# Kernel tuning notes

Measured on AMD Instinct MI355X. Metric: run time of the kernel, lower is better.

## Reference

```python
import jax, jax.numpy as jnp
import numpy as np

EPS = 1e-8  # torch CosineSimilarity eps


def setup_inputs() -> dict:
    key = jax.random.key(0)
    ks = jax.random.split(key, 7)
    B, N, T, C, M, MEM, IN, E = 8, 512, 64, 128, 32, 20, 2, 4
    s = 0.05  # keep softmax logits in a sane range (xavier-like scale)
    return {
        "input": jax.random.normal(ks[0], (B, N, T, IN), jnp.float32),
        "hidden": jax.random.normal(ks[1], (E, B, N, T, C), jnp.float32),
        "memory": jax.random.normal(ks[2], (MEM, M), jnp.float32) * s,
        "input_query": jax.random.normal(ks[3], (IN, M), jnp.float32) * s,
        "Wq": jax.random.normal(ks[4], (E, C, M), jnp.float32) * s,
        "Wk": jax.random.normal(ks[5], (E, C, M), jnp.float32) * s,
        "Wv": jax.random.normal(ks[6], (E, C, M), jnp.float32) * s,
    }


def _cosine_sim(a, b):
    # torch.nn.CosineSimilarity(dim=-1): dot / (max(||a||,eps)*max(||b||,eps))
    num = jnp.sum(a * b, axis=-1)
    na = jnp.maximum(jnp.linalg.norm(a, axis=-1), EPS)
    nb = jnp.maximum(jnp.linalg.norm(b, axis=-1), EPS)
    return num / (na * nb)


def reference(input, hidden, memory, input_query, Wq, Wk, Wv):
    B, N, T, _ = input.shape
    out_dim = 1
    # query_mem: soft read from memory bank -> [B,N,T,mem_hid]
    q_in = jnp.einsum("bnti,im->bntm", input, input_query)
    mem_score = jax.nn.softmax(jnp.einsum("bntm,km->bntk", q_in, memory), axis=-1)
    memories = jnp.einsum("bntk,km->bntm", mem_score, memory)
    # per-expert self-attention over T (vectorized over the 4 experts)
    q = jnp.einsum("ebntc,ecm->ebntm", hidden, Wq)
    k = jnp.einsum("ebntc,ecm->ebntm", hidden, Wk)
    v = jnp.einsum("ebntc,ecm->ebntm", hidden, Wv)
    energy = jnp.einsum("ebntm,ebnsm->ebnts", q, k)  # [E,B,N,T,T]
    att = jnp.einsum("ebnts,ebnsm->ebntm", jax.nn.softmax(energy, axis=-1), v)
    # cosine similarity of memory read vs each expert's attended hidden
    scores = _cosine_sim(memories[None], att)  # [E,B,N,T]
    scores = jnp.moveaxis(scores, 0, -1)  # [B,N,T,E]
    out = jnp.broadcast_to(scores[..., None, :], (B, N, T, out_dim, scores.shape[-1]))
    return out
```

## Files before the change

kernel.cpp:

```cpp
#include <hip/hip_runtime.h>
#include <hip/hip_bf16.h>
#include <math.h>

#define Bc 8
#define Nc 512
#define Tc 64
#define Cc 128
#define Mc 32
#define MEMc 20
#define Ec 4

#define LDK  40
#define LDVT 72

typedef short bf16x8 __attribute__((ext_vector_type(8)));
typedef float f32x4  __attribute__((ext_vector_type(4)));

__device__ __forceinline__ unsigned short f2bfu(float f) {
    return __builtin_bit_cast(unsigned short, __float2bfloat16(f));
}
__device__ __forceinline__ unsigned pk2bf(float x, float y) {
    return ((unsigned)f2bfu(y) << 16) | (unsigned)f2bfu(x);
}

__device__ __forceinline__ void gload_lds16(const void* g, void* l) {
    __builtin_amdgcn_global_load_lds(
        (const __attribute__((address_space(1))) unsigned int*)g,
        (__attribute__((address_space(3))) unsigned int*)l, 16, 0, 0);
}

__global__ void prep(const float* __restrict__ Wq, const float* __restrict__ Wk,
                     const float* __restrict__ Wv, const float* __restrict__ membank,
                     const float* __restrict__ iq,
                     short* __restrict__ wt_img, short* __restrict__ bankM,
                     float* __restrict__ G2) {
    const int t = threadIdx.x;
    if (blockIdx.x < 192) {
        int idx = blockIdx.x * 256 + t;
        int e   = idx / 12288;
        int r   = idx - e * 12288;
        int mat = r >> 12;
        int m   = (r >> 7) & 31;
        int c   = r & 127;
        const float* W = (mat == 0) ? Wq : (mat == 1) ? Wk : Wv;
        const int dst = e * 12288 + mat * 4096 + m * 128 + (c ^ ((m & 7) << 3));
        wt_img[dst] = (short)f2bfu(W[((size_t)e * Cc + c) * Mc + m]);
    } else {
        for (int idx = t; idx < Mc * 32; idx += 256) {
            int m = idx >> 5, k = idx & 31;
            bankM[idx] = (short)f2bfu((k < MEMc) ? membank[k * Mc + m] : 0.f);
        }
        if (t < MEMc) {
            float g0 = 0.f, g1 = 0.f;
            for (int m = 0; m < Mc; ++m) {
                float b = membank[t * Mc + m];
                g0 = fmaf(iq[m], b, g0);
                g1 = fmaf(iq[Mc + m], b, g1);
            }
            G2[2 * t]     = g0;
            G2[2 * t + 1] = g1;
        }
    }
}

__global__ __launch_bounds__(256, 4) void mg_mfma(
    const float* __restrict__ input,
    const float* __restrict__ hidden,
    const short* __restrict__ wt_img,
    const short* __restrict__ bankM,
    const float* __restrict__ G2,
    float* __restrict__ out)
{
    __shared__ __align__(16) short sh_wt[12288];
    __shared__ __align__(16) short sh_k [Tc * LDK];
    __shared__ __align__(16) short sh_vt[Mc * LDVT];

    const int t    = threadIdx.x;
    const int w    = t >> 6;
    const int lane = t & 63;
    const int lo   = lane & 15;
    const int hi   = lane >> 4;
    const int bn   = blockIdx.x & 4095;
    const int e    = blockIdx.x >> 12;

    {
        const short* gsrc = wt_img + (size_t)e * 12288 + w * 512 + lane * 8;
        short* ldst = sh_wt + w * 512;
        #pragma unroll
        for (int c = 0; c < 6; ++c)
            gload_lds16(gsrc + c * 2048, ldst + c * 2048);
    }

    float4 h4[8];
    {
        const float* hrow = hidden + (((size_t)(e * 4096 + bn)) * Tc + w * 16 + lo) * Cc + hi * 8;
        #pragma unroll
        for (int kt = 0; kt < 4; ++kt) {
            h4[2 * kt]     = *(const float4*)(hrow + kt * 32);
            h4[2 * kt + 1] = *(const float4*)(hrow + kt * 32 + 4);
        }
    }
    const float2 in2 = *(const float2*)(input + ((size_t)bn * Tc + lane) * 2);

    unsigned pd[10];
    #pragma unroll
    for (int kp = 0; kp < 10; ++kp) {
        const float4 g = *(const float4*)(G2 + 4 * kp);
        pd[kp] = pk2bf(__expf(in2.x * g.x + in2.y * g.y),
                       __expf(in2.x * g.z + in2.y * g.w));
    }

    bf16x8 a[4];
    #pragma unroll
    for (int kt = 0; kt < 4; ++kt) {
        const float4 x = h4[2 * kt], y = h4[2 * kt + 1];
        uint4 u = (uint4){pk2bf(x.x, x.y), pk2bf(x.z, x.w), pk2bf(y.x, y.y), pk2bf(y.z, y.w)};
        a[kt] = __builtin_bit_cast(bf16x8, u);
    }

    __syncthreads();

    f32x4 q_[2], k_[2], v_[2];
    #pragma unroll
    for (int nt = 0; nt < 2; ++nt) {
        q_[nt] = (f32x4){0.f, 0.f, 0.f, 0.f};
        k_[nt] = (f32x4){0.f, 0.f, 0.f, 0.f};
        v_[nt] = (f32x4){0.f, 0.f, 0.f, 0.f};
    }
    {
        const int swz = (lo & 7) << 3;
        int col[4];
        #pragma unroll
        for (int kt = 0; kt < 4; ++kt) col[kt] = (kt * 32 + hi * 8) ^ swz;
        const short* wrow = sh_wt + lo * 128;
        #pragma unroll
        for (int nt = 0; nt < 2; ++nt) {
            const short* p0 = wrow + nt * 2048;
            #pragma unroll
            for (int kt = 0; kt < 4; ++kt) {
                const bf16x8 aq = *(const bf16x8*)(p0 + col[kt]);
                const bf16x8 ak = *(const bf16x8*)(p0 + 4096 + col[kt]);
                const bf16x8 av = *(const bf16x8*)(p0 + 8192 + col[kt]);
                q_[nt] = __builtin_amdgcn_mfma_f32_16x16x32_bf16(aq, a[kt], q_[nt], 0, 0, 0);
                k_[nt] = __builtin_amdgcn_mfma_f32_16x16x32_bf16(ak, a[kt], k_[nt], 0, 0, 0);
                v_[nt] = __builtin_amdgcn_mfma_f32_16x16x32_bf16(av, a[kt], v_[nt], 0, 0, 0);
            }
        }
    }
    unsigned q_pk[4];
    #pragma unroll
    for (int nt = 0; nt < 2; ++nt) {
        uint2 kw = (uint2){pk2bf(k_[nt][0], k_[nt][1]), pk2bf(k_[nt][2], k_[nt][3])};
        *(uint2*)&sh_k[(w * 16 + lo) * LDK + nt * 16 + hi * 4] = kw;
        #pragma unroll
        for (int j = 0; j < 4; ++j)
            sh_vt[(nt * 16 + hi * 4 + j) * LDVT + w * 16 + lo] = (short)f2bfu(v_[nt][j]);
        q_pk[nt * 2]     = pk2bf(q_[nt][0], q_[nt][1]);
        q_pk[nt * 2 + 1] = pk2bf(q_[nt][2], q_[nt][3]);
    }

    f32x4 am[2];
    am[0] = (f32x4){0.f, 0.f, 0.f, 0.f};
    am[1] = (f32x4){0.f, 0.f, 0.f, 0.f};
    {
        const int addrD = (w * 16 + lo) * 4;
        unsigned Wd[10];
        #pragma unroll
        for (int u = 0; u < 10; ++u)
            Wd[u] = __builtin_amdgcn_ds_bpermute(addrD, (int)pd[u]);
        unsigned b2w[4];
        #pragma unroll
        for (int u = 0; u < 4; ++u) {
            const unsigned lo01 = (hi == 0) ? Wd[u] : Wd[4 + u];
            const unsigned hi23 = (u < 2) ? ((hi == 2) ? Wd[8 + u] : 0u) : 0u;
            b2w[u] = (hi < 2) ? lo01 : hi23;
        }
        const bf16x8 bp2 = __builtin_bit_cast(bf16x8, (uint4){b2w[0], b2w[1], b2w[2], b2w[3]});
        #pragma unroll
        for (int nt = 0; nt < 2; ++nt) {
            const bf16x8 ab = *(const bf16x8*)(bankM + (nt * 16 + lo) * 32 + hi * 8);
            am[nt] = __builtin_amdgcn_mfma_f32_16x16x32_bf16(ab, bp2, am[nt], 0, 0, 0);
        }
    }

    __syncthreads();

    unsigned pw[4][2];
    {
        const int A01 = (((hi & 1) * 32) + lo) << 2;
        const int A23 = A01 + 64;
        unsigned qb0, qb1, qb2, qb3;
        {
            unsigned l0 = __builtin_amdgcn_ds_bpermute(A01, (int)q_pk[0]);
            unsigned h0 = __builtin_amdgcn_ds_bpermute(A01, (int)q_pk[2]);
            unsigned l1 = __builtin_amdgcn_ds_bpermute(A01, (int)q_pk[1]);
            unsigned h1 = __builtin_amdgcn_ds_bpermute(A01, (int)q_pk[3]);
            unsigned l2 = __builtin_amdgcn_ds_bpermute(A23, (int)q_pk[0]);
            unsigned h2 = __builtin_amdgcn_ds_bpermute(A23, (int)q_pk[2]);
            unsigned l3 = __builtin_amdgcn_ds_bpermute(A23, (int)q_pk[1]);
            unsigned h3 = __builtin_amdgcn_ds_bpermute(A23, (int)q_pk[3]);
            qb0 = (hi < 2) ? l0 : h0;
            qb1 = (hi < 2) ? l1 : h1;
            qb2 = (hi < 2) ? l2 : h2;
            qb3 = (hi < 2) ? l3 : h3;
        }
        const bf16x8 bq = __builtin_bit_cast(bf16x8, (uint4){qb0, qb1, qb2, qb3});

        #pragma unroll
        for (int st = 0; st < 4; ++st) {
            const bf16x8 akf = *(const bf16x8*)&sh_k[(st * 16 + lo) * LDK + hi * 8];
            const f32x4 en = __builtin_amdgcn_mfma_f32_16x16x32_bf16(
                akf, bq, (f32x4){0.f, 0.f, 0.f, 0.f}, 0, 0, 0);
            pw[st][0] = pk2bf(__expf(en[0]), __expf(en[1]));
            pw[st][1] = pk2bf(__expf(en[2]), __expf(en[3]));
        }
    }

    f32x4 av[2];
    av[0] = (f32x4){0.f, 0.f, 0.f, 0.f};
    av[1] = (f32x4){0.f, 0.f, 0.f, 0.f};
    {
        const int addrA = (((hi & 1) * 2 + 0) * 16 + lo) * 4;
        const int addrB = (((hi & 1) * 2 + 1) * 16 + lo) * 4;
        bf16x8 bp[2];
        #pragma unroll
        for (int kt = 0; kt < 2; ++kt) {
            unsigned wrd[4];
            #pragma unroll
            for (int u = 0; u < 4; ++u) {
                const int adr = (u < 2) ? addrA : addrB;
                const unsigned ev = __builtin_amdgcn_ds_bpermute(adr, (int)pw[2 * kt][u & 1]);
                const unsigned od = __builtin_amdgcn_ds_bpermute(adr, (int)pw[2 * kt + 1][u & 1]);
                wrd[u] = (hi < 2) ? ev : od;
            }
            bp[kt] = __builtin_bit_cast(bf16x8, (uint4){wrd[0], wrd[1], wrd[2], wrd[3]});
        }
        #pragma unroll
        for (int nt = 0; nt < 2; ++nt)
            #pragma unroll
            for (int kt = 0; kt < 2; ++kt) {
                const bf16x8 avt = *(const bf16x8*)&sh_vt[(nt * 16 + lo) * LDVT + kt * 32 + hi * 8];
                av[nt] = __builtin_amdgcn_mfma_f32_16x16x32_bf16(avt, bp[kt], av[nt], 0, 0, 0);
            }
    }

    {
        float d = 0.f, na = 0.f, nb = 0.f;
        #pragma unroll
        for (int nt = 0; nt < 2; ++nt)
            #pragma unroll
            for (int j = 0; j < 4; ++j) {
                const float av_ = av[nt][j], am_ = am[nt][j];
                d  = fmaf(av_, am_, d);
                na = fmaf(av_, av_, na);
                nb = fmaf(am_, am_, nb);
            }
        d  += __shfl_xor(d, 16);  d  += __shfl_xor(d, 32);
        na += __shfl_xor(na, 16); na += __shfl_xor(na, 32);
        nb += __shfl_xor(nb, 16); nb += __shfl_xor(nb, 32);
        if (hi == 0) {
            const float denom = fmaxf(sqrtf(na), 1e-8f) * fmaxf(sqrtf(nb), 1e-8f);
            out[((size_t)bn * Tc + w * 16 + lo) * Ec + e] = d / denom;
        }
    }
}

extern "C" void kernel_launch(void* const* d_in, const int* in_sizes, int n_in,
                              void* d_out, int out_size, void* d_ws, size_t ws_size,
                              hipStream_t stream) {
    const float* input   = (const float*)d_in[0];
    const float* hidden  = (const float*)d_in[1];
    const float* membank = (const float*)d_in[2];
    const float* iq      = (const float*)d_in[3];
    const float* Wq      = (const float*)d_in[4];
    const float* Wk      = (const float*)d_in[5];
    const float* Wv      = (const float*)d_in[6];
    float* out = (float*)d_out;

    short* wt_img = (short*)d_ws;
    short* bankM  = (short*)((char*)d_ws + 98304);
    float* G2     = (float*)((char*)d_ws + 100352);

    prep<<<193, 256, 0, stream>>>(Wq, Wk, Wv, membank, iq, wt_img, bankM, G2);
    mg_mfma<<<Ec * Bc * Nc, 256, 0, stream>>>(input, hidden, wt_img, bankM, G2, out);
}
```

Measured before the change: 129.8 us.

## Process two (b,n) rows per block to amortize weight staging

Each block now handles two consecutive (b,n) positions for one expert, so the 24KB per-expert weight image loaded into LDS and the bankM fragments are reused across both. The grid is halved, shared K/V buffers are doubled, and launch bounds drop from 4 to 3 blocks per CU to make room for the larger register footprint. The aim is to cut the per-block weight load and launch overhead relative to the streamed hidden data. The cost is higher register pressure and lower occupancy.

```diff
diff --git a/kernel.cpp b/kernel.cpp
--- a/kernel.cpp
+++ b/kernel.cpp
@@ -63,7 +63,7 @@
     }
 }
 
-__global__ __launch_bounds__(256, 4) void mg_mfma(
+__global__ __launch_bounds__(256, 3) void mg_mfma(
     const float* __restrict__ input,
     const float* __restrict__ hidden,
     const short* __restrict__ wt_img,
@@ -72,16 +72,17 @@
     float* __restrict__ out)
 {
     __shared__ __align__(16) short sh_wt[12288];
-    __shared__ __align__(16) short sh_k [Tc * LDK];
-    __shared__ __align__(16) short sh_vt[Mc * LDVT];
+    __shared__ __align__(16) short sh_k [2][Tc * LDK];
+    __shared__ __align__(16) short sh_vt[2][Mc * LDVT];
 
     const int t    = threadIdx.x;
     const int w    = t >> 6;
     const int lane = t & 63;
     const int lo   = lane & 15;
     const int hi   = lane >> 4;
-    const int bn   = blockIdx.x & 4095;
-    const int e    = blockIdx.x >> 12;
+    const int e    = blockIdx.x >> 11;
+    const int bn0  = (blockIdx.x & 2047) * 2;
+    const int bn1  = bn0 + 1;
 
     {
         const short* gsrc = wt_img + (size_t)e * 12288 + w * 512 + lane * 8;
@@ -91,41 +92,80 @@
             gload_lds16(gsrc + c * 2048, ldst + c * 2048);
     }
 
-    float4 h4[8];
+    const float2 in2_0 = *(const float2*)(input + ((size_t)bn0 * Tc + lane) * 2);
+    const float2 in2_1 = *(const float2*)(input + ((size_t)bn1 * Tc + lane) * 2);
+    float4 h0[8], h1[8];
     {
-        const float* hrow = hidden + (((size_t)(e * 4096 + bn)) * Tc + w * 16 + lo) * Cc + hi * 8;
+        const float* hr0 = hidden + (((size_t)(e * 4096 + bn0)) * Tc + w * 16 + lo) * Cc + hi * 8;
+        const float* hr1 = hidden + (((size_t)(e * 4096 + bn1)) * Tc + w * 16 + lo) * Cc + hi * 8;
         #pragma unroll
         for (int kt = 0; kt < 4; ++kt) {
-            h4[2 * kt]     = *(const float4*)(hrow + kt * 32);
-            h4[2 * kt + 1] = *(const float4*)(hrow + kt * 32 + 4);
-        }
-    }
-    const float2 in2 = *(const float2*)(input + ((size_t)bn * Tc + lane) * 2);
-
-    unsigned pd[10];
+            h0[2 * kt]     = *(const float4*)(hr0 + kt * 32);
+            h0[2 * kt + 1] = *(const float4*)(hr0 + kt * 32 + 4);
+            h1[2 * kt]     = *(const float4*)(hr1 + kt * 32);
+            h1[2 * kt + 1] = *(const float4*)(hr1 + kt * 32 + 4);
+        }
+    }
+
+    unsigned pd0[10], pd1[10];
     #pragma unroll
     for (int kp = 0; kp < 10; ++kp) {
         const float4 g = *(const float4*)(G2 + 4 * kp);
-        pd[kp] = pk2bf(__expf(in2.x * g.x + in2.y * g.y),
-                       __expf(in2.x * g.z + in2.y * g.w));
-    }
-
-    bf16x8 a[4];
+        pd0[kp] = pk2bf(__expf(in2_0.x * g.x + in2_0.y * g.y),
+                        __expf(in2_0.x * g.z + in2_0.y * g.w));
+        pd1[kp] = pk2bf(__expf(in2_1.x * g.x + in2_1.y * g.y),
+                        __expf(in2_1.x * g.z + in2_1.y * g.w));
+    }
+
+    f32x4 am0[2], am1[2];
+    am0[0] = am0[1] = (f32x4){0.f, 0.f, 0.f, 0.f};
+    am1[0] = am1[1] = (f32x4){0.f, 0.f, 0.f, 0.f};
+    {
+        const int addrD = (w * 16 + lo) * 4;
+        unsigned W0[10], W1[10];
+        #pragma unroll
+        for (int u = 0; u < 10; ++u) {
+            W0[u] = __builtin_amdgcn_ds_bpermute(addrD, (int)pd0[u]);
+            W1[u] = __builtin_amdgcn_ds_bpermute(addrD, (int)pd1[u]);
+        }
+        unsigned b0[4], b1[4];
+        #pragma unroll
+        for (int u = 0; u < 4; ++u) {
+            const unsigned l0 = (hi == 0) ? W0[u] : W0[4 + u];
+            const unsigned h0_ = (u < 2) ? ((hi == 2) ? W0[8 + u] : 0u) : 0u;
+            b0[u] = (hi < 2) ? l0 : h0_;
+            const unsigned l1 = (hi == 0) ? W1[u] : W1[4 + u];
+            const unsigned h1_ = (u < 2) ? ((hi == 2) ? W1[8 + u] : 0u) : 0u;
+            b1[u] = (hi < 2) ? l1 : h1_;
+        }
+        const bf16x8 bp20 = __builtin_bit_cast(bf16x8, (uint4){b0[0], b0[1], b0[2], b0[3]});
+        const bf16x8 bp21 = __builtin_bit_cast(bf16x8, (uint4){b1[0], b1[1], b1[2], b1[3]});
+        #pragma unroll
+        for (int nt = 0; nt < 2; ++nt) {
+            const bf16x8 ab = *(const bf16x8*)(bankM + (nt * 16 + lo) * 32 + hi * 8);
+            am0[nt] = __builtin_amdgcn_mfma_f32_16x16x32_bf16(ab, bp20, am0[nt], 0, 0, 0);
+            am1[nt] = __builtin_amdgcn_mfma_f32_16x16x32_bf16(ab, bp21, am1[nt], 0, 0, 0);
+        }
+    }
+
+    bf16x8 a0[4], a1[4];
     #pragma unroll
     for (int kt = 0; kt < 4; ++kt) {
-        const float4 x = h4[2 * kt], y = h4[2 * kt + 1];
-        uint4 u = (uint4){pk2bf(x.x, x.y), pk2bf(x.z, x.w), pk2bf(y.x, y.y), pk2bf(y.z, y.w)};
-        a[kt] = __builtin_bit_cast(bf16x8, u);
+        const float4 x0 = h0[2 * kt], y0 = h0[2 * kt + 1];
+        a0[kt] = __builtin_bit_cast(bf16x8, (uint4){pk2bf(x0.x, x0.y), pk2bf(x0.z, x0.w),
+                                                    pk2bf(y0.x, y0.y), pk2bf(y0.z, y0.w)});
+        const float4 x1 = h1[2 * kt], y1 = h1[2 * kt + 1];
+        a1[kt] = __builtin_bit_cast(bf16x8, (uint4){pk2bf(x1.x, x1.y), pk2bf(x1.z, x1.w),
+                                                    pk2bf(y1.x, y1.y), pk2bf(y1.z, y1.w)});
     }
 
     __syncthreads();
 
-    f32x4 q_[2], k_[2], v_[2];
+    f32x4 q0_[2], k0_[2], v0_[2], q1_[2], k1_[2], v1_[2];
     #pragma unroll
     for (int nt = 0; nt < 2; ++nt) {
-        q_[nt] = (f32x4){0.f, 0.f, 0.f, 0.f};
-        k_[nt] = (f32x4){0.f, 0.f, 0.f, 0.f};
-        v_[nt] = (f32x4){0.f, 0.f, 0.f, 0.f};
+        q0_[nt] = k0_[nt] = v0_[nt] = (f32x4){0.f, 0.f, 0.f, 0.f};
+        q1_[nt] = k1_[nt] = v1_[nt] = (f32x4){0.f, 0.f, 0.f, 0.f};
     }
     {
         const int swz = (lo & 7) << 3;
@@ -138,113 +178,97 @@
             const short* p0 = wrow + nt * 2048;
             #pragma unroll
             for (int kt = 0; kt < 4; ++kt) {
-                const bf16x8 aq = *(const bf16x8*)(p0 + col[kt]);
-                const bf16x8 ak = *(const bf16x8*)(p0 + 4096 + col[kt]);
-                const bf16x8 av = *(const bf16x8*)(p0 + 8192 + col[kt]);
-                q_[nt] = __builtin_amdgcn_mfma_f32_16x16x32_bf16(aq, a[kt], q_[nt], 0, 0, 0);
-                k_[nt] = __builtin_amdgcn_mfma_f32_16x16x32_bf16(ak, a[kt], k_[nt], 0, 0, 0);
-                v_[nt] = __builtin_amdgcn_mfma_f32_16x16x32_bf16(av, a[kt], v_[nt], 0, 0, 0);
-            }
-        }
-    }
-    unsigned q_pk[4];
+                const bf16x8 wq = *(const bf16x8*)(p0 + col[kt]);
+                const bf16x8 wk = *(const bf16x8*)(p0 + 4096 + col[kt]);
+                const bf16x8 wv = *(const bf16x8*)(p0 + 8192 + col[kt]);
+                q0_[nt] = __builtin_amdgcn_mfma_f32_16x16x32_bf16(wq, a0[kt], q0_[nt], 0, 0, 0);
+                k0_[nt] = __builtin_amdgcn_mfma_f32_16x16x32_bf16(wk, a0[kt], k0_[nt], 0, 0, 0);
+                v0_[nt] = __builtin_amdgcn_mfma_f32_16x16x32_bf16(wv, a0[kt], v0_[nt], 0, 0, 0);
+                q1_[nt] = __builtin_amdgcn_mfma_f32_16x16x32_bf16(wq, a1[kt], q1_[nt], 0, 0, 0);
+                k1_[nt] = __builtin_amdgcn_mfma_f32_16x16x32_bf16(wk, a1[kt], k1_[nt], 0, 0, 0);
+                v1_[nt] = __builtin_amdgcn_mfma_f32_16x16x32_bf16(wv, a1[kt], v1_[nt], 0, 0, 0);
+            }
+        }
+    }
+    unsigned q_pk0[4], q_pk1[4];
     #pragma unroll
     for (int nt = 0; nt < 2; ++nt) {
-        uint2 kw = (uint2){pk2bf(k_[nt][0], k_[nt][1]), pk2bf(k_[nt][2], k_[nt][3])};
-        *(uint2*)&sh_k[(w * 16 + lo) * LDK + nt * 16 + hi * 4] = kw;
-        #pragma unroll
-        for (int j = 0; j < 4; ++j)
-            sh_vt[(nt * 16 + hi * 4 + j) * LDVT + w * 16 + lo] = (short)f2bfu(v_[nt][j]);
-        q_pk[nt * 2]     = pk2bf(q_[nt][0], q_[nt][1]);
-        q_pk[nt * 2 + 1] = pk2bf(q_[nt][2], q_[nt][3]);
-    }
-
-    f32x4 am[2];
-    am[0] = (f32x4){0.f, 0.f, 0.f, 0.f};
-    am[1] = (f32x4){0.f, 0.f, 0.f, 0.f};
-    {
-        const int addrD = (w * 16 + lo) * 4;
-        unsigned Wd[10];
-        #pragma unroll
-        for (int u = 0; u < 10; ++u)
-            Wd[u] = __builtin_amdgcn_ds_bpermute(addrD, (int)pd[u]);
-        unsigned b2w[4];
-        #pragma unroll
-        for (int u = 0; u < 4; ++u) {
-            const unsigned lo01 = (hi == 0) ? Wd[u] : Wd[4 + u];
-            const unsigned hi23 = (u < 2) ? ((hi == 2) ? Wd[8 + u] : 0u) : 0u;
-            b2w[u] = (hi < 2) ? lo01 : hi23;
-        }
-        const bf16x8 bp2 = __builtin_bit_cast(bf16x8, (uint4){b2w[0], b2w[1], b2w[2], b2w[3]});
-        #pragma unroll
-        for (int nt = 0; nt < 2; ++nt) {
-            const bf16x8 ab = *(const bf16x8*)(bankM + (nt * 16 + lo) * 32 + hi * 8);
-            am[nt] = __builtin_amdgcn_mfma_f32_16x16x32_bf16(ab, bp2, am[nt], 0, 0, 0);
-        }
+        *(uint2*)&sh_k[0][(w * 16 + lo) * LDK + nt * 16 + hi * 4] =
+            (uint2){pk2bf(k0_[nt][0], k0_[nt][1]), pk2bf(k0_[nt][2], k0_[nt][3])};
+        *(uint2*)&sh_k[1][(w * 16 + lo) * LDK + nt * 16 + hi * 4] =
+            (uint2){pk2bf(k1_[nt][0], k1_[nt][1]), pk2bf(k1_[nt][2], k1_[nt][3])};
+        #pragma unroll
+        for (int j = 0; j < 4; ++j) {
+            sh_vt[0][(nt * 16 + hi * 4 + j) * LDVT + w * 16 + lo] = (short)f2bfu(v0_[nt][j]);
+            sh_vt[1][(nt * 16 + hi * 4 + j) * LDVT + w * 16 + lo] = (short)f2bfu(v1_[nt][j]);
+        }
+        q_pk0[nt * 2]     = pk2bf(q0_[nt][0], q0_[nt][1]);
+        q_pk0[nt * 2 + 1] = pk2bf(q0_[nt][2], q0_[nt][3]);
+        q_pk1[nt * 2]     = pk2bf(q1_[nt][0], q1_[nt][1]);
+        q_pk1[nt * 2 + 1] = pk2bf(q1_[nt][2], q1_[nt][3]);
     }
 
     __syncthreads();
 
-    unsigned pw[4][2];
-    {
-        const int A01 = (((hi & 1) * 32) + lo) << 2;
-        const int A23 = A01 + 64;
-        unsigned qb0, qb1, qb2, qb3;
+    const int A01   = (((hi & 1) * 32) + lo) << 2;
+    const int A23   = A01 + 64;
+    const int addrA = (((hi & 1) * 2 + 0) * 16 + lo) * 4;
+    const int addrB = (((hi & 1) * 2 + 1) * 16 + lo) * 4;
+
+    #pragma unroll
+    for (int u = 0; u < 2; ++u) {
+        const unsigned* q_pk = u ? q_pk1 : q_pk0;
+        const f32x4*    am   = u ? am1   : am0;
+        const int       bn   = u ? bn1   : bn0;
+
+        unsigned pw[4][2];
         {
             unsigned l0 = __builtin_amdgcn_ds_bpermute(A01, (int)q_pk[0]);
-            unsigned h0 = __builtin_amdgcn_ds_bpermute(A01, (int)q_pk[2]);
+            unsigned h0_ = __builtin_amdgcn_ds_bpermute(A01, (int)q_pk[2]);
             unsigned l1 = __builtin_amdgcn_ds_bpermute(A01, (int)q_pk[1]);
-            unsigned h1 = __builtin_amdgcn_ds_bpermute(A01, (int)q_pk[3]);
+            unsigned h1_ = __builtin_amdgcn_ds_bpermute(A01, (int)q_pk[3]);
             unsigned l2 = __builtin_amdgcn_ds_bpermute(A23, (int)q_pk[0]);
-            unsigned h2 = __builtin_amdgcn_ds_bpermute(A23, (int)q_pk[2]);
+            unsigned h2_ = __builtin_amdgcn_ds_bpermute(A23, (int)q_pk[2]);
             unsigned l3 = __builtin_amdgcn_ds_bpermute(A23, (int)q_pk[1]);
-            unsigned h3 = __builtin_amdgcn_ds_bpermute(A23, (int)q_pk[3]);
-            qb0 = (hi < 2) ? l0 : h0;
-            qb1 = (hi < 2) ? l1 : h1;
-            qb2 = (hi < 2) ? l2 : h2;
-            qb3 = (hi < 2) ? l3 : h3;
-        }
-        const bf16x8 bq = __builtin_bit_cast(bf16x8, (uint4){qb0, qb1, qb2, qb3});
-
-        #pragma unroll
-        for (int st = 0; st < 4; ++st) {
-            const bf16x8 akf = *(const bf16x8*)&sh_k[(st * 16 + lo) * LDK + hi * 8];
-            const f32x4 en = __builtin_amdgcn_mfma_f32_16x16x32_bf16(
-                akf, bq, (f32x4){0.f, 0.f, 0.f, 0.f}, 0, 0, 0);
-            pw[st][0] = pk2bf(__expf(en[0]), __expf(en[1]));
-            pw[st][1] = pk2bf(__expf(en[2]), __expf(en[3]));
-        }
-    }
-
-    f32x4 av[2];
-    av[0] = (f32x4){0.f, 0.f, 0.f, 0.f};
-    av[1] = (f32x4){0.f, 0.f, 0.f, 0.f};
-    {
-        const int addrA = (((hi & 1) * 2 + 0) * 16 + lo) * 4;
-        const int addrB = (((hi & 1) * 2 + 1) * 16 + lo) * 4;
-        bf16x8 bp[2];
-        #pragma unroll
-        for (int kt = 0; kt < 2; ++kt) {
-            unsigned wrd[4];
-            #pragma unroll
-            for (int u = 0; u < 4; ++u) {
-                const int adr = (u < 2) ? addrA : addrB;
-                const unsigned ev = __builtin_amdgcn_ds_bpermute(adr, (int)pw[2 * kt][u & 1]);
-                const unsigned od = __builtin_amdgcn_ds_bpermute(adr, (int)pw[2 * kt + 1][u & 1]);
-                wrd[u] = (hi < 2) ? ev : od;
-            }
-            bp[kt] = __builtin_bit_cast(bf16x8, (uint4){wrd[0], wrd[1], wrd[2], wrd[3]});
-        }
-        #pragma unroll
-        for (int nt = 0; nt < 2; ++nt)
+            unsigned h3_ = __builtin_amdgcn_ds_bpermute(A23, (int)q_pk[3]);
+            const bf16x8 bq = __builtin_bit_cast(bf16x8, (uint4){
+                (hi < 2) ? l0 : h0_, (hi < 2) ? l1 : h1_,
+                (hi < 2) ? l2 : h2_, (hi < 2) ? l3 : h3_});
+            #pragma unroll
+            for (int st = 0; st < 4; ++st) {
+                const bf16x8 akf = *(const bf16x8*)&sh_k[u][(st * 16 + lo) * LDK + hi * 8];
+                const f32x4 en = __builtin_amdgcn_mfma_f32_16x16x32_bf16(
+                    akf, bq, (f32x4){0.f, 0.f, 0.f, 0.f}, 0, 0, 0);
+                pw[st][0] = pk2bf(__expf(en[0]), __expf(en[1]));
+                pw[st][1] = pk2bf(__expf(en[2]), __expf(en[3]));
+            }
+        }
+
+        f32x4 av[2];
+        av[0] = av[1] = (f32x4){0.f, 0.f, 0.f, 0.f};
+        {
+            bf16x8 bp[2];
             #pragma unroll
             for (int kt = 0; kt < 2; ++kt) {
-                const bf16x8 avt = *(const bf16x8*)&sh_vt[(nt * 16 + lo) * LDVT + kt * 32 + hi * 8];
-                av[nt] = __builtin_amdgcn_mfma_f32_16x16x32_bf16(avt, bp[kt], av[nt], 0, 0, 0);
-            }
-    }
-
-    {
+                unsigned wrd[4];
+                #pragma unroll
+                for (int uu = 0; uu < 4; ++uu) {
+                    const int adr = (uu < 2) ? addrA : addrB;
+                    const unsigned ev = __builtin_amdgcn_ds_bpermute(adr, (int)pw[2 * kt][uu & 1]);
+                    const unsigned od = __builtin_amdgcn_ds_bpermute(adr, (int)pw[2 * kt + 1][uu & 1]);
+                    wrd[uu] = (hi < 2) ? ev : od;
+                }
+                bp[kt] = __builtin_bit_cast(bf16x8, (uint4){wrd[0], wrd[1], wrd[2], wrd[3]});
+            }
+            #pragma unroll
+            for (int nt = 0; nt < 2; ++nt)
+                #pragma unroll
+                for (int kt = 0; kt < 2; ++kt) {
+                    const bf16x8 avt = *(const bf16x8*)&sh_vt[u][(nt * 16 + lo) * LDVT + kt * 32 + hi * 8];
+                    av[nt] = __builtin_amdgcn_mfma_f32_16x16x32_bf16(avt, bp[kt], av[nt], 0, 0, 0);
+                }
+        }
+
         float d = 0.f, na = 0.f, nb = 0.f;
         #pragma unroll
         for (int nt = 0; nt < 2; ++nt)
@@ -282,5 +306,5 @@
     float* G2     = (float*)((char*)d_ws + 100352);
 
     prep<<<193, 256, 0, stream>>>(Wq, Wk, Wv, membank, iq, wt_img, bankM, G2);
-    mg_mfma<<<Ec * Bc * Nc, 256, 0, stream>>>(input, hidden, wt_img, bankM, G2, out);
-}
+    mg_mfma<<<Ec * Bc * Nc / 2, 256, 0, stream>>>(input, hidden, wt_img, bankM, G2, out);
+}
```

Result: faster. 122.8 us (-5.3%).
